# Kernel tuning notes

Measured on AMD Instinct MI355X. Metric: run time of the kernel, lower is better.

Reference implementation:

```python
import jax, jax.numpy as jnp
import numpy as np

EMB, HEAD = 2048, 128

def setup_inputs() -> dict:
    key = jax.random.key(0)
    ks = jax.random.split(key, 7)
    x = jax.random.normal(ks[0], (4, 4096, EMB), dtype=jnp.float32)
    s = 1.0 / np.sqrt(EMB)
    wK = jax.random.normal(ks[1], (EMB, HEAD), dtype=jnp.float32) * s
    bK = jax.random.normal(ks[2], (HEAD,), dtype=jnp.float32) * 0.01
    wQ = jax.random.normal(ks[3], (EMB, HEAD), dtype=jnp.float32) * s
    bQ = jax.random.normal(ks[4], (HEAD,), dtype=jnp.float32) * 0.01
    wV = jax.random.normal(ks[5], (EMB, HEAD), dtype=jnp.float32) * s
    bV = jax.random.normal(ks[6], (HEAD,), dtype=jnp.float32) * 0.01
    return {"x": x, "wK": wK, "bK": bK, "wQ": wQ, "bQ": bQ, "wV": wV, "bV": bV}

def reference(x, wK, bK, wQ, bQ, wV, bV):
    B, S, E = x.shape
    K = x @ wK + bK                      # [B,S,H]
    Q = x @ wQ + bQ
    V = x @ wV + bV
    scale = 1.0 / jnp.sqrt(jnp.float32(HEAD))
    att = jnp.einsum('bqh,bkh->bqk', Q, K) * scale   # [B,S,S]
    causal = jnp.tril(jnp.ones((S, S), dtype=bool))
    att = jnp.where(causal, att, -jnp.inf)
    att = jax.nn.softmax(att, axis=-1)
    return jnp.einsum('bqk,bkh->bqh', att, V)        # [B,S,H]
```

## Files before the change

### kernel.cpp

```cpp
#include <hip/hip_runtime.h>
#include <hip/hip_bf16.h>
#include <math.h>

#define SEQ  4096
#define BATCH 4
#define EMBD 2048
#define HDIM 128

#define SCALE_LOG2E 0.12753102721944556f

typedef __bf16 bf16x8 __attribute__((ext_vector_type(8)));
typedef __bf16 bf16x4 __attribute__((ext_vector_type(4)));
typedef float  f32x4  __attribute__((ext_vector_type(4)));

__device__ __forceinline__ bf16x8 ldfrag(const __bf16* p) {
    return *(const bf16x8*)p;
}

__device__ __forceinline__ void gl_lds16(const __bf16* g, __bf16* l) {
    __builtin_amdgcn_global_load_lds(
        (const __attribute__((address_space(1))) void*)g,
        (__attribute__((address_space(3))) void*)l, 16, 0, 0);
}

__global__ __launch_bounds__(256)
void cvt_w(const float* __restrict__ wQ, const float* __restrict__ wK,
           const float* __restrict__ wV, __bf16* __restrict__ wt) {
    const float* w = (blockIdx.z == 0) ? wQ : (blockIdx.z == 1) ? wK : wV;
    __bf16* dst = wt + (size_t)blockIdx.z * HDIM * EMBD;
    int k0 = blockIdx.x * 32;
    int n0 = blockIdx.y * 32;
    __shared__ float t[32][33];
    {
        int r  = threadIdx.x >> 3;
        int c4 = (threadIdx.x & 7) * 4;
        float4 v = *(const float4*)(w + (size_t)(k0 + r) * HDIM + n0 + c4);
        t[r][c4 + 0] = v.x; t[r][c4 + 1] = v.y;
        t[r][c4 + 2] = v.z; t[r][c4 + 3] = v.w;
    }
    __syncthreads();
    {
        int n  = threadIdx.x >> 3;
        int k4 = (threadIdx.x & 7) * 4;
        bf16x4 o = { (__bf16)t[k4 + 0][n], (__bf16)t[k4 + 1][n],
                     (__bf16)t[k4 + 2][n], (__bf16)t[k4 + 3][n] };
        *(bf16x4*)(dst + (size_t)(n0 + n) * EMBD + k0 + k4) = o;
    }
}

__global__ __launch_bounds__(512, 2)
void proj(const float* __restrict__ x,
          const __bf16* __restrict__ wt,
          const float* __restrict__ bQ, const float* __restrict__ bK,
          const float* __restrict__ bV,
          __bf16* __restrict__ qws, __bf16* __restrict__ kws,
          __bf16* __restrict__ vtws) {
    const int m0   = blockIdx.x * 64;
    const int w    = threadIdx.x >> 6;
    const int lane = threadIdx.x & 63;
    const int ln   = lane & 15;
    const int quad = lane >> 4;
    const int lr   = lane >> 3;
    const int lc   = lane & 7;

    __shared__ __bf16 smem[57344];

    const float* gX = x + (size_t)(m0 + w * 8 + lr) * EMBD + lc * 8;
    const __bf16* gB = wt + (size_t)(w * 48 + lr) * EMBD + (lc ^ lr) * 8;

    const f32x4 fzero = {0.f, 0.f, 0.f, 0.f};
    f32x4 acc[4][3];
#pragma unroll
    for (int i = 0; i < 4; i++)
#pragma unroll
        for (int j = 0; j < 3; j++) acc[i][j] = fzero;

    float4 a0, a1;
    auto loadA = [&](int k0) {
        a0 = *(const float4*)(gX + k0);
        a1 = *(const float4*)(gX + k0 + 4);
    };
    auto writeA = [&](int buf) {
        bf16x8 o = { (__bf16)a0.x, (__bf16)a0.y, (__bf16)a0.z, (__bf16)a0.w,
                     (__bf16)a1.x, (__bf16)a1.y, (__bf16)a1.z, (__bf16)a1.w };
        __bf16* lA = smem + buf * 28672;
        *(bf16x8*)(lA + (w * 8 + lr) * 64 + ((lc ^ lr) * 8)) = o;
    };
    auto stageB = [&](int buf, int k0) {
        __bf16* lB = smem + buf * 28672 + 4096;
#pragma unroll
        for (int i = 0; i < 6; i++)
            gl_lds16(gB + (size_t)(i * 8) * EMBD + k0,
                     lB + (w * 48 + i * 8) * 64);
    };

    auto compute = [&](int buf) {
        const __bf16* lA = smem + buf * 28672;
        const __bf16* lB = lA + 4096;
#pragma unroll
        for (int kk = 0; kk < 2; kk++) {
            bf16x8 a[4], bb[3];
#pragma unroll
            for (int i = 0; i < 4; i++)
                a[i] = ldfrag(lA + (i * 16 + ln) * 64 +
                              (((quad + 4 * kk) ^ (ln & 7)) * 8));
#pragma unroll
            for (int j = 0; j < 3; j++)
                bb[j] = ldfrag(lB + (w * 48 + j * 16 + ln) * 64 +
                               (((quad + 4 * kk) ^ (ln & 7)) * 8));
#pragma unroll
            for (int i = 0; i < 4; i++)
#pragma unroll
                for (int j = 0; j < 3; j++)
                    acc[i][j] = __builtin_amdgcn_mfma_f32_16x16x32_bf16(
                        a[i], bb[j], acc[i][j], 0, 0, 0);
        }
    };

    loadA(0);
    stageB(0, 0);
    writeA(0);
    __syncthreads();
    for (int t = 0; t < 32; t++) {
        const int cur = t & 1;
        if (t < 31) {
            loadA((t + 1) * 64);
            stageB(cur ^ 1, (t + 1) * 64);
        }
        compute(cur);
        if (t < 31) writeA(cur ^ 1);
        __syncthreads();
    }

    __bf16* so = smem;
    constexpr int SOS = 392;
#pragma unroll
    for (int j = 0; j < 3; j++) {
        int c = w * 48 + j * 16 + ln;
        const float* bp = (c < 128) ? bQ : (c < 256) ? bK : bV;
        float bv = bp[c & 127];
#pragma unroll
        for (int i = 0; i < 4; i++)
#pragma unroll
            for (int r = 0; r < 4; r++)
                so[(i * 16 + quad * 4 + r) * SOS + c] =
                    (__bf16)(acc[i][j][r] + bv);
    }
    __syncthreads();

    {
        int row = threadIdx.x >> 3;
        int c0  = (threadIdx.x & 7) * 32;
        __bf16* dst = (c0 < 128)
            ? qws + (size_t)(m0 + row) * HDIM + c0
            : kws + (size_t)(m0 + row) * HDIM + (c0 - 128);
#pragma unroll
        for (int k = 0; k < 4; k++)
            *(bf16x8*)(dst + k * 8) =
                *(const bf16x8*)(so + row * SOS + c0 + k * 8);
    }
    {
        int h   = threadIdx.x >> 2;
        int sc  = (threadIdx.x & 3) * 16;
        int bb2 = m0 >> 12;
        int s0g = m0 & (SEQ - 1);
        bf16x8 o0, o1;
#pragma unroll
        for (int ss = 0; ss < 8; ss++)
            o0[ss] = so[(sc + ss) * SOS + 256 + h];
#pragma unroll
        for (int ss = 0; ss < 8; ss++)
            o1[ss] = so[(sc + 8 + ss) * SOS + 256 + h];
        __bf16* dst = vtws + ((size_t)bb2 * HDIM + h) * SEQ + s0g + sc;
        *(bf16x8*)dst = o0;
        *(bf16x8*)(dst + 8) = o1;
    }
}

__global__ __launch_bounds__(256, 2)
void attn(const __bf16* __restrict__ qws, const __bf16* __restrict__ kws,
          const __bf16* __restrict__ vtws,
          float* __restrict__ Opart, float* __restrict__ Lpart) {
    const int blk = blockIdx.x;
    const int b   = (blk & 7) >> 1;
    int wi = ((blk >> 3) << 1) | (blk & 1);
    wi = 287 - wi;
    int a = (int)((sqrtf((float)wi + 1.0f) - 1.0f) * 0.5f);
    while (4 * (a + 1) * (a + 2) <= wi) a++;
    while (a > 0 && 4 * a * (a + 1) > wi) a--;
    const int rem = wi - 4 * a * (a + 1);
    const int qt  = a * 8 + rem / (a + 1);
    const int c   = rem - (rem / (a + 1)) * (a + 1);
    const int q0  = qt * 64;
    const int kt0 = c * 8;
    const int kt1 = (kt0 + 8 < qt + 1) ? (kt0 + 8) : (qt + 1);
    const int slot = b * 288 + wi;

    const int wv   = threadIdx.x >> 6;
    const int lane = threadIdx.x & 63;
    const int ln   = lane & 15;
    const int quad = lane >> 4;

    __shared__ __bf16 lK[2][64 * 128];
    __shared__ __bf16 lV[2][128 * 64];
    __shared__ __bf16 lP[4][16 * 72];

    const __bf16* kws_b = kws + (size_t)b * SEQ * HDIM;
    const __bf16* vt_b  = vtws + (size_t)b * HDIM * SEQ;

    const __bf16* qbase =
        qws + ((size_t)(b * SEQ) + q0 + wv * 16 + ln) * HDIM + quad * 8;
    bf16x8 qf[4];
#pragma unroll
    for (int kk = 0; kk < 4; kk++) qf[kk] = ldfrag(qbase + kk * 32);

    const f32x4 fzero = {0.f, 0.f, 0.f, 0.f};
    float lrun[4];
    f32x4 oacc[8];
#pragma unroll
    for (int r = 0; r < 4; r++) lrun[r] = 0.f;
#pragma unroll
    for (int j = 0; j < 8; j++) oacc[j] = fzero;

    const int krow_i = lane >> 4, kslot = lane & 15;
    const int vrow_i = lane >> 3, vslot = lane & 7;

    auto stageK = [&](int k0, int buf) {
#pragma unroll
        for (int i = 0; i < 4; i++) {
            int row = wv * 16 + i * 4 + krow_i;
            const __bf16* src = kws_b + (size_t)(k0 + row) * HDIM +
                                ((kslot ^ (row & 7)) * 8);
            gl_lds16(src, &lK[buf][(wv * 16 + i * 4) * 128]);
        }
    };
    auto stageV = [&](int k0, int buf) {
#pragma unroll
        for (int i = 0; i < 4; i++) {
            int row = wv * 32 + i * 8 + vrow_i;
            const __bf16* src = vt_b + (size_t)row * SEQ + k0 +
                                ((vslot ^ (row & 7)) * 8);
            gl_lds16(src, &lV[buf][(wv * 32 + i * 8) * 64]);
        }
    };

    stageK(kt0 * 64, 0);
    stageV(kt0 * 64, 0);

    for (int kt = kt0; kt < kt1; kt++) {
        __syncthreads();
        const int cur = (kt - kt0) & 1;
        if (kt + 1 < kt1) {
            stageK((kt + 1) * 64, cur ^ 1);
            stageV((kt + 1) * 64, cur ^ 1);
        }

        f32x4 sacc[4];
#pragma unroll
        for (int j = 0; j < 4; j++) sacc[j] = fzero;
        const __bf16* Kb = lK[cur];
#pragma unroll
        for (int j = 0; j < 4; j++) {
#pragma unroll
            for (int kk = 0; kk < 4; kk++) {
                bf16x8 kf = ldfrag(Kb + (j * 16 + ln) * 128 +
                                   (((quad + 4 * kk) ^ (ln & 7)) * 8));
                sacc[j] = __builtin_amdgcn_mfma_f32_16x16x32_bf16(
                    qf[kk], kf, sacc[j], 0, 0, 0);
            }
        }

        const bool diag = (kt == qt);
#pragma unroll
        for (int j = 0; j < 4; j++) {
#pragma unroll
            for (int r = 0; r < 4; r++) {
                float p = exp2f(sacc[j][r] * SCALE_LOG2E);
                if (diag) {
                    int col = kt * 64 + j * 16 + ln;
                    int row = q0 + wv * 16 + quad * 4 + r;
                    if (col > row) p = 0.f;
                }
                lrun[r] += p;
                lP[wv][(quad * 4 + r) * 72 + j * 16 + ln] = (__bf16)p;
            }
        }

        __builtin_amdgcn_s_waitcnt(0xc07f);
        bf16x8 af0 = ldfrag(&lP[wv][ln * 72 + quad * 8]);
        bf16x8 af1 = ldfrag(&lP[wv][ln * 72 + 32 + quad * 8]);

        const __bf16* Vb = lV[cur];
#pragma unroll
        for (int j = 0; j < 8; j++) {
            bf16x8 v0 = ldfrag(Vb + (j * 16 + ln) * 64 +
                               ((quad ^ (ln & 7)) * 8));
            bf16x8 v1 = ldfrag(Vb + (j * 16 + ln) * 64 +
                               (((quad + 4) ^ (ln & 7)) * 8));
            oacc[j] = __builtin_amdgcn_mfma_f32_16x16x32_bf16(
                af0, v0, oacc[j], 0, 0, 0);
            oacc[j] = __builtin_amdgcn_mfma_f32_16x16x32_bf16(
                af1, v1, oacc[j], 0, 0, 0);
        }
    }

#pragma unroll
    for (int r = 0; r < 4; r++) {
#pragma unroll
        for (int off = 8; off >= 1; off >>= 1)
            lrun[r] += __shfl_xor(lrun[r], off);
    }
    if (ln == 0) {
#pragma unroll
        for (int r = 0; r < 4; r++)
            Lpart[(size_t)slot * 64 + wv * 16 + quad * 4 + r] = lrun[r];
    }
    float* Ob = Opart + (size_t)slot * 8192;
#pragma unroll
    for (int r = 0; r < 4; r++) {
        int row = wv * 16 + quad * 4 + r;
#pragma unroll
        for (int j = 0; j < 8; j++)
            Ob[(size_t)row * 128 + j * 16 + ln] = oacc[j][r];
    }
}

__global__ __launch_bounds__(256)
void attn_fin(const float* __restrict__ Opart, const float* __restrict__ Lpart,
              float* __restrict__ out) {
    const int b  = blockIdx.x >> 6;
    const int qt = blockIdx.x & 63;
    const int a  = qt >> 3;
    const int nch = a + 1;
    const int base = b * 288 + 4 * a * (a + 1) + (qt & 7) * (a + 1);
    const int row = threadIdx.x >> 2;
    const int c0  = (threadIdx.x & 3) * 32;

    float l = 0.f;
    f32x4 o[8];
#pragma unroll
    for (int i = 0; i < 8; i++) o[i] = {0.f, 0.f, 0.f, 0.f};
    for (int ch = 0; ch < nch; ch++) {
        const f32x4* Op = (const f32x4*)(Opart + (size_t)(base + ch) * 8192 +
                                         (size_t)row * 128 + c0);
        l += Lpart[(size_t)(base + ch) * 64 + row];
#pragma unroll
        for (int i = 0; i < 8; i++) o[i] += Op[i];
    }
    float inv = 1.f / l;
    f32x4* orow = (f32x4*)(out + ((size_t)(b * SEQ) + qt * 64 + row) * HDIM + c0);
#pragma unroll
    for (int i = 0; i < 8; i++) orow[i] = o[i] * inv;
}

extern "C" void kernel_launch(void* const* d_in, const int* in_sizes, int n_in,
                              void* d_out, int out_size, void* d_ws,
                              size_t ws_size, hipStream_t stream) {
    const float* x  = (const float*)d_in[0];
    const float* wK = (const float*)d_in[1];
    const float* bK = (const float*)d_in[2];
    const float* wQ = (const float*)d_in[3];
    const float* bQ = (const float*)d_in[4];
    const float* wV = (const float*)d_in[5];
    const float* bV = (const float*)d_in[6];
    float* out = (float*)d_out;

    __bf16* wt   = (__bf16*)d_ws;
    __bf16* qws  = wt + (size_t)3 * HDIM * EMBD;
    __bf16* kws  = qws + (size_t)BATCH * SEQ * HDIM;
    __bf16* vtws = kws + (size_t)BATCH * SEQ * HDIM;
    float* Opart = (float*)(vtws + (size_t)BATCH * SEQ * HDIM);
    float* Lpart = Opart + (size_t)1152 * 8192;

    hipLaunchKernelGGL(cvt_w, dim3(EMBD / 32, HDIM / 32, 3), dim3(256), 0,
                       stream, wQ, wK, wV, wt);
    hipLaunchKernelGGL(proj, dim3(SEQ * BATCH / 64), dim3(512), 0, stream,
                       x, wt, bQ, bK, bV, qws, kws, vtws);
    hipLaunchKernelGGL(attn, dim3(1152), dim3(256), 0, stream,
                       qws, kws, vtws, Opart, Lpart);
    hipLaunchKernelGGL(attn_fin, dim3(256), dim3(256), 0, stream,
                       Opart, Lpart, out);
}
```

Baseline: 280.2 us.

## Load K/V MFMA fragments directly from global memory, dropping LDS staging

Removes the double-buffered LDS staging of K and V tiles, the async global-to-LDS copies and the per-iteration block barrier. Each wave now reads its MFMA fragments straight from global memory, relying on L1/L2 to absorb the fourfold redundancy across waves. With LDS freed, the occupancy hint rises to 3 blocks per CU, and s_setprio brackets the MFMA loops. The trade is more global/L2 traffic and exposed load latency with no software prefetch, in exchange for higher occupancy and no synchronisation.

```diff
diff --git a/kernel.cpp b/kernel.cpp
--- a/kernel.cpp
+++ b/kernel.cpp
@@ -177,7 +177,7 @@
     }
 }
 
-__global__ __launch_bounds__(256, 2)
+__global__ __launch_bounds__(256, 3)
 void attn(const __bf16* __restrict__ qws, const __bf16* __restrict__ kws,
           const __bf16* __restrict__ vtws,
           float* __restrict__ Opart, float* __restrict__ Lpart) {
@@ -201,8 +201,6 @@
     const int ln   = lane & 15;
     const int quad = lane >> 4;
 
-    __shared__ __bf16 lK[2][64 * 128];
-    __shared__ __bf16 lV[2][128 * 64];
     __shared__ __bf16 lP[4][16 * 72];
 
     const __bf16* kws_b = kws + (size_t)b * SEQ * HDIM;
@@ -214,6 +212,9 @@
 #pragma unroll
     for (int kk = 0; kk < 4; kk++) qf[kk] = ldfrag(qbase + kk * 32);
 
+    const __bf16* kfb = kws_b + (size_t)ln * HDIM + quad * 8;
+    const __bf16* vfb = vt_b + (size_t)ln * SEQ + quad * 8;
+
     const f32x4 fzero = {0.f, 0.f, 0.f, 0.f};
     float lrun[4];
     f32x4 oacc[8];
@@ -222,53 +223,24 @@
 #pragma unroll
     for (int j = 0; j < 8; j++) oacc[j] = fzero;
 
-    const int krow_i = lane >> 4, kslot = lane & 15;
-    const int vrow_i = lane >> 3, vslot = lane & 7;
-
-    auto stageK = [&](int k0, int buf) {
-#pragma unroll
-        for (int i = 0; i < 4; i++) {
-            int row = wv * 16 + i * 4 + krow_i;
-            const __bf16* src = kws_b + (size_t)(k0 + row) * HDIM +
-                                ((kslot ^ (row & 7)) * 8);
-            gl_lds16(src, &lK[buf][(wv * 16 + i * 4) * 128]);
-        }
-    };
-    auto stageV = [&](int k0, int buf) {
-#pragma unroll
-        for (int i = 0; i < 4; i++) {
-            int row = wv * 32 + i * 8 + vrow_i;
-            const __bf16* src = vt_b + (size_t)row * SEQ + k0 +
-                                ((vslot ^ (row & 7)) * 8);
-            gl_lds16(src, &lV[buf][(wv * 32 + i * 8) * 64]);
-        }
-    };
-
-    stageK(kt0 * 64, 0);
-    stageV(kt0 * 64, 0);
-
     for (int kt = kt0; kt < kt1; kt++) {
-        __syncthreads();
-        const int cur = (kt - kt0) & 1;
-        if (kt + 1 < kt1) {
-            stageK((kt + 1) * 64, cur ^ 1);
-            stageV((kt + 1) * 64, cur ^ 1);
-        }
+        const int k0 = kt * 64;
 
         f32x4 sacc[4];
 #pragma unroll
         for (int j = 0; j < 4; j++) sacc[j] = fzero;
-        const __bf16* Kb = lK[cur];
+        __builtin_amdgcn_s_setprio(1);
 #pragma unroll
         for (int j = 0; j < 4; j++) {
 #pragma unroll
             for (int kk = 0; kk < 4; kk++) {
-                bf16x8 kf = ldfrag(Kb + (j * 16 + ln) * 128 +
-                                   (((quad + 4 * kk) ^ (ln & 7)) * 8));
+                bf16x8 kf = ldfrag(kfb + (size_t)(k0 + j * 16) * HDIM +
+                                   kk * 32);
                 sacc[j] = __builtin_amdgcn_mfma_f32_16x16x32_bf16(
                     qf[kk], kf, sacc[j], 0, 0, 0);
             }
         }
+        __builtin_amdgcn_s_setprio(0);
 
         const bool diag = (kt == qt);
 #pragma unroll
@@ -277,7 +249,7 @@
             for (int r = 0; r < 4; r++) {
                 float p = exp2f(sacc[j][r] * SCALE_LOG2E);
                 if (diag) {
-                    int col = kt * 64 + j * 16 + ln;
+                    int col = k0 + j * 16 + ln;
                     int row = q0 + wv * 16 + quad * 4 + r;
                     if (col > row) p = 0.f;
                 }
@@ -290,18 +262,18 @@
         bf16x8 af0 = ldfrag(&lP[wv][ln * 72 + quad * 8]);
         bf16x8 af1 = ldfrag(&lP[wv][ln * 72 + 32 + quad * 8]);
 
-        const __bf16* Vb = lV[cur];
+        __builtin_amdgcn_s_setprio(1);
 #pragma unroll
         for (int j = 0; j < 8; j++) {
-            bf16x8 v0 = ldfrag(Vb + (j * 16 + ln) * 64 +
-                               ((quad ^ (ln & 7)) * 8));
-            bf16x8 v1 = ldfrag(Vb + (j * 16 + ln) * 64 +
-                               (((quad + 4) ^ (ln & 7)) * 8));
+            const __bf16* vj = vfb + (size_t)(j * 16) * SEQ + k0;
+            bf16x8 v0 = ldfrag(vj);
+            bf16x8 v1 = ldfrag(vj + 32);
             oacc[j] = __builtin_amdgcn_mfma_f32_16x16x32_bf16(
                 af0, v0, oacc[j], 0, 0, 0);
             oacc[j] = __builtin_amdgcn_mfma_f32_16x16x32_bf16(
                 af1, v1, oacc[j], 0, 0, 0);
         }
+        __builtin_amdgcn_s_setprio(0);
     }
 
 #pragma unroll
```

New measurement: 403.8 us. +44.1%, slower.
